# Optimization experiments

Hardware: AMD Instinct MI355X
Metric: run time of the kernel (lower is better)

## Reference

```python
import jax, jax.numpy as jnp
import numpy as np

CODE_NUM = 100000
GRAPH = 256
HIDDEN = 256
TIME = 256


def gru_cell(x, h, w_ih, w_hh, b_ih, b_hh):
    # torch.nn.GRUCell math. x:[N,G] h:[N,H] w_ih:[3H,G] w_hh:[3H,H]
    gi = x @ w_ih.T + b_ih
    gh = h @ w_hh.T + b_hh
    i_r, i_z, i_n = jnp.split(gi, 3, axis=-1)
    h_r, h_z, h_n = jnp.split(gh, 3, axis=-1)
    r = jax.nn.sigmoid(i_r + h_r)
    z = jax.nn.sigmoid(i_z + h_z)
    n = jnp.tanh(i_n + r * h_n)
    return (1.0 - z) * n + z * h


def setup_inputs() -> dict:
    key = jax.random.key(0)
    ks = jax.random.split(key, 12)
    s_ih = 1.0 / np.sqrt(HIDDEN)
    return {
        "interval": jax.random.uniform(ks[0], (1,), jnp.float32) * 100.0 + 1.0,
        "t": 0,
        "co_embeddings": jax.random.normal(ks[1], (CODE_NUM, GRAPH), jnp.float32),
        "divided": jax.random.randint(ks[2], (CODE_NUM, 3), 0, 2, jnp.int32),
        "no_embeddings": jax.random.normal(ks[3], (1, GRAPH), jnp.float32),
        "unrelated_embeddings": jax.random.normal(ks[4], (1, GRAPH), jnp.float32),
        "is_last": 0,
        "hidden_state": jax.random.normal(ks[5], (CODE_NUM, HIDDEN), jnp.float32),
        "weight_ih": jax.random.uniform(ks[6], (3 * HIDDEN, GRAPH), jnp.float32, -s_ih, s_ih),
        "weight_hh": jax.random.uniform(ks[7], (3 * HIDDEN, HIDDEN), jnp.float32, -s_ih, s_ih),
        "bias_ih": jax.random.uniform(ks[8], (3 * HIDDEN,), jnp.float32, -s_ih, s_ih),
        "bias_hh": jax.random.uniform(ks[9], (3 * HIDDEN,), jnp.float32, -s_ih, s_ih),
        "time_w": jax.random.normal(ks[10], (TIME, 1), jnp.float32) * 0.02,
        "time_b": jax.random.normal(ks[11], (TIME,), jnp.float32) * 0.02,
    }


def reference(interval, t, co_embeddings, divided, no_embeddings,
              unrelated_embeddings, is_last, hidden_state,
              weight_ih, weight_hh, bias_ih, bias_hh, time_w, time_b):
    # time branch: tanh(Linear(1/log(interval + e)))
    inv = 1.0 / jnp.log(interval[:, None] + jnp.exp(jnp.float32(1.0)))  # [1,1]
    time_features = jnp.tanh(inv @ time_w.T + time_b)                  # [1,TIME]

    # not is_last branch: gather rows where any of divided[:,0:3] > 0,
    # run GRUCell, scatter into zeros, max-reduce over selected rows.
    # Masked formulation is row-wise exact (GRUCell acts per row).
    mask = jnp.any(divided > 0, axis=1)                                 # [N]
    h_all = gru_cell(co_embeddings, hidden_state,
                     weight_ih, weight_hh, bias_ih, bias_hh)            # [N,H]
    h_new = jnp.where(mask[:, None], h_all, 0.0)                        # scatter into zeros
    output = jnp.max(jnp.where(mask[:, None], h_all, -jnp.inf), axis=0) # max over gathered rows, [H]
    return output + time_features, h_new
```

## Files before the change

### kernel.cpp

```cpp
#include <hip/hip_runtime.h>
#include <hip/hip_bf16.h>
#include <math.h>

#define M_ROWS 100000
#define ROWS_PER_XCD 12500
#define NTILES 49
#define NCHUNK 49152

typedef __attribute__((ext_vector_type(8)))  short  short8;
typedef __attribute__((ext_vector_type(16))) float  float16v;

__device__ __forceinline__ unsigned short bf16_rne(float f) {
    unsigned u = __builtin_bit_cast(unsigned, f);
    u += 0x7FFFu + ((u >> 16) & 1u);
    return (unsigned short)(u >> 16);
}

__device__ __forceinline__ float sigmoid_fast(float x) {
    return 1.0f / (1.0f + __expf(-x));
}
__device__ __forceinline__ float tanh_fast(float x) {
    return 1.0f - 2.0f / (__expf(2.0f * x) + 1.0f);
}

__device__ __forceinline__ unsigned pack2_rn(float lo, float hi) {
    __hip_bfloat162 t = __float22bfloat162_rn(float2{lo, hi});
    unsigned u;
    __builtin_memcpy(&u, &t, 4);
    return u;
}

__device__ __forceinline__ short8 pack_bf16x8(float4 a, float4 b) {
    union { short8 s; unsigned u[4]; } r;
    r.u[0] = pack2_rn(a.x, a.y);
    r.u[1] = pack2_rn(a.z, a.w);
    r.u[2] = pack2_rn(b.x, b.y);
    r.u[3] = pack2_rn(b.z, b.w);
    return r.s;
}

__global__ void prep_kernel(const float* __restrict__ wih,
                            const float* __restrict__ whh,
                            const int* __restrict__ divided,
                            unsigned short* __restrict__ wswz,
                            unsigned int* __restrict__ maxacc,
                            int* __restrict__ maskbuf)
{
    int idx = blockIdx.x * 256 + threadIdx.x;
    if (idx < NCHUNK) {
        int lane = idx & 63;
        int t    = idx >> 6;
        int s    = t % 6;
        int t2   = t / 6;
        int kc   = t2 & 15;
        int g    = t2 >> 4;
        int row  = (s % 3) * 256 + g * 32 + (lane & 31);
        int col  = kc * 16 + (lane >> 5) * 8;
        const float* src = (s < 3 ? wih : whh) + row * 256 + col;
        float4 a = reinterpret_cast<const float4*>(src)[0];
        float4 b = reinterpret_cast<const float4*>(src)[1];
        uint4 p;
        p.x = (unsigned)bf16_rne(a.x) | ((unsigned)bf16_rne(a.y) << 16);
        p.y = (unsigned)bf16_rne(a.z) | ((unsigned)bf16_rne(a.w) << 16);
        p.z = (unsigned)bf16_rne(b.x) | ((unsigned)bf16_rne(b.y) << 16);
        p.w = (unsigned)bf16_rne(b.z) | ((unsigned)bf16_rne(b.w) << 16);
        reinterpret_cast<uint4*>(wswz)[idx] = p;
    } else if (idx < NCHUNK + M_ROWS) {
        int m = idx - NCHUNK;
        maskbuf[m] = (divided[3 * m] > 0) | (divided[3 * m + 1] > 0) | (divided[3 * m + 2] > 0);
    } else if (idx < NCHUNK + M_ROWS + 256) {
        maxacc[idx - NCHUNK - M_ROWS] = 0u;
    }
}

__global__ __launch_bounds__(512, 2) void gru_main(
    const float* __restrict__ X,
    const float* __restrict__ H,
    const unsigned short* __restrict__ Wswz,
    const float* __restrict__ bih,
    const float* __restrict__ bhh,
    const int* __restrict__ maskbuf,
    float* __restrict__ hnew,
    unsigned int* __restrict__ maxacc)
{
    __shared__ unsigned short Wlds[NCHUNK];

    const int tid  = threadIdx.x;
    const int lane = tid & 63;
    const int wave = tid >> 6;
    const int l32  = lane & 31;
    const int hi   = lane >> 5;

    const int b    = blockIdx.x;
    const int xcd  = b & 7;
    const int slot = b >> 3;
    const int g    = slot & 7;
    const int sub  = slot >> 3;
    const int base  = xcd * ROWS_PER_XCD;
    const int limit = base + ROWS_PER_XCD;

    {
        const uint4* ws = reinterpret_cast<const uint4*>(Wswz) + (size_t)g * 6144;
        uint4* wd = reinterpret_cast<uint4*>(Wlds);
        #pragma unroll
        for (int i = 0; i < 12; ++i) wd[i * 512 + tid] = ws[i * 512 + tid];
    }
    __syncthreads();

    const short8* wbase = reinterpret_cast<const short8*>(Wlds);
    const int jj = g * 32 + l32;
    const float bir = bih[jj], biz = bih[256 + jj], bin_ = bih[512 + jj];
    const float bhr = bhh[jj], bhz = bhh[256 + jj], bhn  = bhh[512 + jj];

    float colmax = -__builtin_inff();

    for (int t = sub; t < NTILES; t += 4) {
        const int wrow0 = base + t * 256 + wave * 32;
        if (wrow0 >= limit) continue;
        const int arow = min(wrow0 + l32, limit - 1);
        const float4* X4 = reinterpret_cast<const float4*>(X) + (size_t)arow * 64;
        const float4* H4 = reinterpret_cast<const float4*>(H) + (size_t)arow * 64;

        float16v acc[6];
        #pragma unroll
        for (int s = 0; s < 6; ++s)
            #pragma unroll
            for (int q = 0; q < 16; ++q) acc[s][q] = 0.0f;

        float4 xb[2][4], hb[2][4];
        #pragma unroll
        for (int c = 0; c < 2; ++c)
            #pragma unroll
            for (int f = 0; f < 2; ++f) {
                int fi = c * 4 + hi * 2 + f;
                xb[0][c * 2 + f] = X4[fi];
                hb[0][c * 2 + f] = H4[fi];
            }

        #pragma unroll
        for (int q = 0; q < 8; ++q) {
            const int cur = q & 1, nxt = cur ^ 1;
            if (q < 7) {
                #pragma unroll
                for (int c = 0; c < 2; ++c)
                    #pragma unroll
                    for (int f = 0; f < 2; ++f) {
                        int fi = (q * 2 + 2 + c) * 4 + hi * 2 + f;
                        xb[nxt][c * 2 + f] = X4[fi];
                        hb[nxt][c * 2 + f] = H4[fi];
                    }
            }
            short8 ax[2], ah[2];
            #pragma unroll
            for (int c = 0; c < 2; ++c) {
                ax[c] = pack_bf16x8(xb[cur][c * 2], xb[cur][c * 2 + 1]);
                ah[c] = pack_bf16x8(hb[cur][c * 2], hb[cur][c * 2 + 1]);
            }
            #pragma unroll
            for (int c = 0; c < 2; ++c) {
                const int kc = q * 2 + c;
                const short8* wk = wbase + (kc * 6) * 64 + lane;
                acc[0] = __builtin_amdgcn_mfma_f32_32x32x16_bf16(ax[c], wk[0],   acc[0], 0, 0, 0);
                acc[1] = __builtin_amdgcn_mfma_f32_32x32x16_bf16(ax[c], wk[64],  acc[1], 0, 0, 0);
                acc[2] = __builtin_amdgcn_mfma_f32_32x32x16_bf16(ax[c], wk[128], acc[2], 0, 0, 0);
                acc[3] = __builtin_amdgcn_mfma_f32_32x32x16_bf16(ah[c], wk[192], acc[3], 0, 0, 0);
                acc[4] = __builtin_amdgcn_mfma_f32_32x32x16_bf16(ah[c], wk[256], acc[4], 0, 0, 0);
                acc[5] = __builtin_amdgcn_mfma_f32_32x32x16_bf16(ah[c], wk[320], acc[5], 0, 0, 0);
            }
        }

        #pragma unroll
        for (int reg = 0; reg < 16; ++reg) {
            int rl = (reg & 3) + 8 * (reg >> 2) + 4 * hi;
            int m  = wrow0 + rl;
            if (m < limit) {
                float gir = acc[0][reg] + bir;
                float giz = acc[1][reg] + biz;
                float gin = acc[2][reg] + bin_;
                float ghr = acc[3][reg] + bhr;
                float ghz = acc[4][reg] + bhz;
                float ghn = acc[5][reg] + bhn;
                float r = sigmoid_fast(gir + ghr);
                float z = sigmoid_fast(giz + ghz);
                float n = tanh_fast(gin + r * ghn);
                float hp = H[(size_t)m * 256 + jj];
                float hv = (1.0f - z) * n + z * hp;
                int mk = maskbuf[m];
                __builtin_nontemporal_store(mk ? hv : 0.0f, &hnew[(size_t)m * 256 + jj]);
                if (mk) colmax = fmaxf(colmax, hv);
            }
        }
    }

    colmax = fmaxf(colmax, __shfl_xor(colmax, 32));
    if (hi == 0) {
        unsigned bb = __builtin_bit_cast(unsigned, colmax);
        unsigned u  = (bb & 0x80000000u) ? ~bb : (bb | 0x80000000u);
        atomicMax(&maxacc[jj], u);
    }
}

__global__ void finalize_kernel(const unsigned int* __restrict__ maxacc,
                                const float* __restrict__ interval,
                                const float* __restrict__ time_w,
                                const float* __restrict__ time_b,
                                float* __restrict__ out)
{
    int j = threadIdx.x;
    unsigned u = maxacc[j];
    unsigned b = (u & 0x80000000u) ? (u & 0x7FFFFFFFu) : ~u;
    float mx = __builtin_bit_cast(float, b);
    float inv = 1.0f / logf(interval[0] + 2.718281828459045f);
    out[j] = mx + tanhf(inv * time_w[j] + time_b[j]);
}

extern "C" void kernel_launch(void* const* d_in, const int* in_sizes, int n_in,
                              void* d_out, int out_size, void* d_ws, size_t ws_size,
                              hipStream_t stream) {
    const float* interval = (const float*)d_in[0];
    const float* co       = (const float*)d_in[2];
    const int*   divided  = (const int*)d_in[3];
    const float* hidden   = (const float*)d_in[7];
    const float* wih      = (const float*)d_in[8];
    const float* whh      = (const float*)d_in[9];
    const float* bih      = (const float*)d_in[10];
    const float* bhh      = (const float*)d_in[11];
    const float* time_w   = (const float*)d_in[12];
    const float* time_b   = (const float*)d_in[13];

    float* out  = (float*)d_out;
    float* hnew = out + 256;

    unsigned short* wswz   = (unsigned short*)d_ws;
    unsigned int*   maxacc = (unsigned int*)((char*)d_ws + 786432);
    int*            maskbuf= (int*)((char*)d_ws + 786432 + 1024);

    int prep_elems  = NCHUNK + M_ROWS + 256;
    int prep_blocks = (prep_elems + 255) / 256;

    prep_kernel<<<prep_blocks, 256, 0, stream>>>(wih, whh, divided, wswz, maxacc, maskbuf);

    gru_main<<<256, 512, 0, stream>>>(co, hidden, wswz,
                                      bih, bhh, maskbuf, hnew, maxacc);

    finalize_kernel<<<1, 256, 0, stream>>>(maxacc, interval, time_w, time_b, out);
}
```

Before: 523.8 us.

## Pre-pack activations to bf16 MFMA layout and fuse finalize via last-block counter

A prep pass converts X and H into a bf16 buffer laid out in MFMA operand order, so the main kernel loads pre-swizzled short8 fragments directly. Those fragments are prefetched four k-steps ahead into registers. The finalize kernel is folded into the main kernel using an atomic done-counter, which removes one launch. In exchange, the prep pass reads all of X and H and writes about 100MB of packed data, which adds memory traffic, and the path only runs when the workspace is large enough.

```diff
diff --git a/kernel.cpp b/kernel.cpp
--- a/kernel.cpp
+++ b/kernel.cpp
@@ -3,6 +3,9 @@
 #include <math.h>
 
 #define M_ROWS 100000
+#define NGROUPS 3125
+#define NTILES_TOTAL 391
+#define TILES_PER_XCD 49
 #define ROWS_PER_XCD 12500
 #define NTILES 49
 #define NCHUNK 49152
@@ -39,15 +42,43 @@
     return r.s;
 }
 
-__global__ void prep_kernel(const float* __restrict__ wih,
+__global__ void prep_kernel(const float* __restrict__ X,
+                            const float* __restrict__ H,
+                            const float* __restrict__ wih,
                             const float* __restrict__ whh,
                             const int* __restrict__ divided,
                             unsigned short* __restrict__ wswz,
+                            unsigned short* __restrict__ apack,
                             unsigned int* __restrict__ maxacc,
-                            int* __restrict__ maskbuf)
+                            int* __restrict__ maskbuf,
+                            unsigned int* __restrict__ donecnt,
+                            int pack_blocks)
 {
-    int idx = blockIdx.x * 256 + threadIdx.x;
-    if (idx < NCHUNK) {
+    const int b   = blockIdx.x;
+    const int tid = threadIdx.x;
+
+    if (b < pack_blocks) {
+        int gt   = b * 256 + tid;
+        int lane = gt & 63;
+        int u    = gt >> 6;
+        int gr   = u >> 4;
+        int kc   = u & 15;
+        int row  = gr * 32 + (lane & 31);
+        int col  = kc * 16 + (lane >> 5) * 8;
+        const float* xs = X + (size_t)row * 256 + col;
+        const float* hs = H + (size_t)row * 256 + col;
+        float4 a = reinterpret_cast<const float4*>(xs)[0];
+        float4 c = reinterpret_cast<const float4*>(xs)[1];
+        reinterpret_cast<short8*>(apack)[(size_t)(u * 2) * 64 + lane] = pack_bf16x8(a, c);
+        float4 d = reinterpret_cast<const float4*>(hs)[0];
+        float4 e = reinterpret_cast<const float4*>(hs)[1];
+        reinterpret_cast<short8*>(apack)[(size_t)(u * 2 + 1) * 64 + lane] = pack_bf16x8(d, e);
+        return;
+    }
+
+    int bb = b - pack_blocks;
+    if (bb < 192) {
+        int idx  = bb * 256 + tid;
         int lane = idx & 63;
         int t    = idx >> 6;
         int s    = t % 6;
@@ -58,22 +89,153 @@
         int col  = kc * 16 + (lane >> 5) * 8;
         const float* src = (s < 3 ? wih : whh) + row * 256 + col;
         float4 a = reinterpret_cast<const float4*>(src)[0];
-        float4 b = reinterpret_cast<const float4*>(src)[1];
+        float4 c = reinterpret_cast<const float4*>(src)[1];
         uint4 p;
         p.x = (unsigned)bf16_rne(a.x) | ((unsigned)bf16_rne(a.y) << 16);
         p.y = (unsigned)bf16_rne(a.z) | ((unsigned)bf16_rne(a.w) << 16);
-        p.z = (unsigned)bf16_rne(b.x) | ((unsigned)bf16_rne(b.y) << 16);
-        p.w = (unsigned)bf16_rne(b.z) | ((unsigned)bf16_rne(b.w) << 16);
+        p.z = (unsigned)bf16_rne(c.x) | ((unsigned)bf16_rne(c.y) << 16);
+        p.w = (unsigned)bf16_rne(c.z) | ((unsigned)bf16_rne(c.w) << 16);
         reinterpret_cast<uint4*>(wswz)[idx] = p;
-    } else if (idx < NCHUNK + M_ROWS) {
-        int m = idx - NCHUNK;
-        maskbuf[m] = (divided[3 * m] > 0) | (divided[3 * m + 1] > 0) | (divided[3 * m + 2] > 0);
-    } else if (idx < NCHUNK + M_ROWS + 256) {
-        maxacc[idx - NCHUNK - M_ROWS] = 0u;
-    }
-}
-
-__global__ __launch_bounds__(512, 2) void gru_main(
+    } else if (bb < 192 + 391) {
+        int m = (bb - 192) * 256 + tid;
+        if (m < M_ROWS)
+            maskbuf[m] = (divided[3 * m] > 0) | (divided[3 * m + 1] > 0) | (divided[3 * m + 2] > 0);
+    } else {
+        maxacc[tid] = 0u;
+        if (tid == 0) *donecnt = 0u;
+    }
+}
+
+__global__ __launch_bounds__(512, 2) void gru_main_packed(
+    const unsigned short* __restrict__ Apack,
+    const float* __restrict__ H,
+    const unsigned short* __restrict__ Wswz,
+    const float* __restrict__ bih,
+    const float* __restrict__ bhh,
+    const int* __restrict__ maskbuf,
+    const float* __restrict__ interval,
+    const float* __restrict__ time_w,
+    const float* __restrict__ time_b,
+    float* __restrict__ hnew,
+    unsigned int* __restrict__ maxacc,
+    unsigned int* __restrict__ donecnt,
+    float* __restrict__ out)
+{
+    __shared__ unsigned short Wlds[49152];
+    __shared__ int islast;
+
+    const int tid  = threadIdx.x;
+    const int lane = tid & 63;
+    const int wave = tid >> 6;
+    const int l32  = lane & 31;
+    const int hi   = lane >> 5;
+
+    const int b    = blockIdx.x;
+    const int xcd  = b & 7;
+    const int slot = b >> 3;
+    const int g    = slot & 7;
+    const int sub  = slot >> 3;
+
+    const int tbeg = xcd * TILES_PER_XCD + sub;
+    const int tend = min(xcd * TILES_PER_XCD + TILES_PER_XCD, NTILES_TOTAL);
+
+    {
+        const uint4* ws = reinterpret_cast<const uint4*>(Wswz) + (size_t)g * 6144;
+        uint4* wd = reinterpret_cast<uint4*>(Wlds);
+        #pragma unroll
+        for (int i = 0; i < 12; ++i) wd[i * 512 + tid] = ws[i * 512 + tid];
+    }
+    __syncthreads();
+
+    const short8* wbase = reinterpret_cast<const short8*>(Wlds);
+    const short8* A8b   = reinterpret_cast<const short8*>(Apack);
+    const int jj = g * 32 + l32;
+    const float bir = bih[jj], biz = bih[256 + jj], bin_ = bih[512 + jj];
+    const float bhr = bhh[jj], bhz = bhh[256 + jj], bhn  = bhh[512 + jj];
+
+    float colmax = -__builtin_inff();
+
+    for (int t = tbeg; t < tend; t += 4) {
+        const int wrow0 = t * 256 + wave * 32;
+        if (wrow0 >= M_ROWS) continue;
+        const int gr0 = wrow0 >> 5;
+        const short8* A8 = A8b + (size_t)gr0 * 2048 + lane;
+
+        float16v acc[6];
+        #pragma unroll
+        for (int s = 0; s < 6; ++s)
+            #pragma unroll
+            for (int q = 0; q < 16; ++q) acc[s][q] = 0.0f;
+
+        short8 bx[4], bh[4];
+        #pragma unroll
+        for (int p = 0; p < 4; ++p) {
+            bx[p] = A8[p * 128];
+            bh[p] = A8[p * 128 + 64];
+        }
+
+        #pragma unroll
+        for (int kc = 0; kc < 16; ++kc) {
+            const int cur = kc & 3;
+            const short8 ax = bx[cur];
+            const short8 ah = bh[cur];
+            if (kc < 12) {
+                bx[cur] = A8[(kc + 4) * 128];
+                bh[cur] = A8[(kc + 4) * 128 + 64];
+            }
+            const short8* wk = wbase + kc * 384 + lane;
+            acc[0] = __builtin_amdgcn_mfma_f32_32x32x16_bf16(ax, wk[0],   acc[0], 0, 0, 0);
+            acc[1] = __builtin_amdgcn_mfma_f32_32x32x16_bf16(ax, wk[64],  acc[1], 0, 0, 0);
+            acc[2] = __builtin_amdgcn_mfma_f32_32x32x16_bf16(ax, wk[128], acc[2], 0, 0, 0);
+            acc[3] = __builtin_amdgcn_mfma_f32_32x32x16_bf16(ah, wk[192], acc[3], 0, 0, 0);
+            acc[4] = __builtin_amdgcn_mfma_f32_32x32x16_bf16(ah, wk[256], acc[4], 0, 0, 0);
+            acc[5] = __builtin_amdgcn_mfma_f32_32x32x16_bf16(ah, wk[320], acc[5], 0, 0, 0);
+        }
+
+        #pragma unroll
+        for (int reg = 0; reg < 16; ++reg) {
+            const int rl = (reg & 3) + 8 * (reg >> 2) + 4 * hi;
+            const int m  = wrow0 + rl;
+            float gir = acc[0][reg] + bir;
+            float giz = acc[1][reg] + biz;
+            float gin = acc[2][reg] + bin_;
+            float ghr = acc[3][reg] + bhr;
+            float ghz = acc[4][reg] + bhz;
+            float ghn = acc[5][reg] + bhn;
+            float r = sigmoid_fast(gir + ghr);
+            float z = sigmoid_fast(giz + ghz);
+            float n = tanh_fast(gin + r * ghn);
+            float hp = H[(size_t)m * 256 + jj];
+            float hv = (1.0f - z) * n + z * hp;
+            int mk = maskbuf[m];
+            __builtin_nontemporal_store(mk ? hv : 0.0f, &hnew[(size_t)m * 256 + jj]);
+            if (mk) colmax = fmaxf(colmax, hv);
+        }
+    }
+
+    colmax = fmaxf(colmax, __shfl_xor(colmax, 32));
+    if (hi == 0) {
+        unsigned bb = __builtin_bit_cast(unsigned, colmax);
+        unsigned u  = (bb & 0x80000000u) ? ~bb : (bb | 0x80000000u);
+        atomicMax(&maxacc[jj], u);
+    }
+
+    __syncthreads();
+    if (tid == 0) {
+        __threadfence();
+        islast = (atomicAdd(donecnt, 1u) == 255u) ? 1 : 0;
+    }
+    __syncthreads();
+    if (islast && tid < 256) {
+        unsigned u  = atomicMax(&maxacc[tid], 0u);
+        unsigned bb2 = (u & 0x80000000u) ? (u & 0x7FFFFFFFu) : ~u;
+        float mx  = __builtin_bit_cast(float, bb2);
+        float inv = 1.0f / logf(interval[0] + 2.718281828459045f);
+        out[tid]  = mx + tanhf(inv * time_w[tid] + time_b[tid]);
+    }
+}
+
+__global__ __launch_bounds__(512, 2) void gru_main_legacy(
     const float* __restrict__ X,
     const float* __restrict__ H,
     const unsigned short* __restrict__ Wswz,
@@ -231,17 +393,27 @@
     float* out  = (float*)d_out;
     float* hnew = out + 256;
 
-    unsigned short* wswz   = (unsigned short*)d_ws;
-    unsigned int*   maxacc = (unsigned int*)((char*)d_ws + 786432);
-    int*            maskbuf= (int*)((char*)d_ws + 786432 + 1024);
-
-    int prep_elems  = NCHUNK + M_ROWS + 256;
-    int prep_blocks = (prep_elems + 255) / 256;
-
-    prep_kernel<<<prep_blocks, 256, 0, stream>>>(wih, whh, divided, wswz, maxacc, maskbuf);
-
-    gru_main<<<256, 512, 0, stream>>>(co, hidden, wswz,
-                                      bih, bhh, maskbuf, hnew, maxacc);
-
-    finalize_kernel<<<1, 256, 0, stream>>>(maxacc, interval, time_w, time_b, out);
-}
+    unsigned short* wswz    = (unsigned short*)d_ws;
+    unsigned int*   maxacc  = (unsigned int*)((char*)d_ws + 786432);
+    int*            maskbuf = (int*)((char*)d_ws + 787456);
+    unsigned int*   donecnt = (unsigned int*)((char*)d_ws + 1187456);
+    unsigned short* apack   = (unsigned short*)((char*)d_ws + 2097152);
+
+    const size_t NEED = 2097152ull + 102400000ull;
+    const bool packed = (ws_size >= NEED);
+    const int pb = packed ? 12500 : 0;
+
+    prep_kernel<<<pb + 584, 256, 0, stream>>>(co, hidden, wih, whh, divided,
+                                              wswz, apack, maxacc, maskbuf,
+                                              donecnt, pb);
+
+    if (packed) {
+        gru_main_packed<<<256, 512, 0, stream>>>(apack, hidden, wswz, bih, bhh,
+                                                 maskbuf, interval, time_w, time_b,
+                                                 hnew, maxacc, donecnt, out);
+    } else {
+        gru_main_legacy<<<256, 512, 0, stream>>>(co, hidden, wswz,
+                                                 bih, bhh, maskbuf, hnew, maxacc);
+        finalize_kernel<<<1, 256, 0, stream>>>(maxacc, interval, time_w, time_b, out);
+    }
+}
```

Result: faster. 459.0 us (-12.4%).
